# Kernel tuning notes

Measured on AMD Instinct MI355X. Metric: run time of the kernel, lower is better.

## Reference

```python
import jax, jax.numpy as jnp
import numpy as np

D_MODEL = 2048
N_HEADS = 16
HEAD_DIM = D_MODEL // N_HEADS
SEQ = 2048
THETA = 10000.0


def rope_tables(head_dim, context_length, theta=THETA):
    inv_freq = 1.0 / theta ** (jnp.arange(0, head_dim, 2, dtype=jnp.float32) / head_dim)
    angles = jnp.arange(context_length, dtype=jnp.float32)[:, None] * inv_freq[None, :]
    angles = jnp.concatenate([angles, angles], axis=1)  # [S, head_dim]
    return jnp.cos(angles), jnp.sin(angles)


def apply_rope(x, cos, sin):
    # x: [B, H, S, Dh]; cos/sin: [S, Dh]
    half = x.shape[-1] // 2
    x1, x2 = x[..., :half], x[..., half:]
    rotated = jnp.concatenate([-x2, x1], axis=-1)
    return x * cos[None, None] + rotated * sin[None, None]


def setup_inputs() -> dict:
    key = jax.random.key(0)
    ks = jax.random.split(key, 5)
    s = 1.0 / np.sqrt(D_MODEL)
    x = jax.random.normal(ks[0], (2, SEQ, D_MODEL), dtype=jnp.float32)
    Wq = jax.random.normal(ks[1], (D_MODEL, D_MODEL), dtype=jnp.float32) * s
    Wk = jax.random.normal(ks[2], (D_MODEL, D_MODEL), dtype=jnp.float32) * s
    Wv = jax.random.normal(ks[3], (D_MODEL, D_MODEL), dtype=jnp.float32) * s
    Wo = jax.random.normal(ks[4], (D_MODEL, D_MODEL), dtype=jnp.float32) * s
    return {"x": x, "Wq": Wq, "Wk": Wk, "Wv": Wv, "Wo": Wo}


def reference(x, Wq, Wk, Wv, Wo):
    B, S, D = x.shape
    cos, sin = rope_tables(HEAD_DIM, SEQ)
    cos, sin = cos[:S], sin[:S]

    def split_heads(t):  # [B,S,D] -> [B,H,S,Dh]
        return t.reshape(B, S, N_HEADS, HEAD_DIM).transpose(0, 2, 1, 3)

    q = apply_rope(split_heads(x @ Wq.T), cos, sin)
    k = apply_rope(split_heads(x @ Wk.T), cos, sin)
    v = split_heads(x @ Wv.T)

    scores = jnp.einsum('bhqd,bhkd->bhqk', q, k) / np.sqrt(HEAD_DIM).astype(np.float32)
    causal = jnp.tril(jnp.ones((S, S), dtype=bool))
    scores = jnp.where(causal[None, None], scores, -jnp.inf)
    weights = jax.nn.softmax(scores, axis=-1)
    ctx = jnp.einsum('bhqk,bhkd->bhqd', weights, v)
    ctx = ctx.transpose(0, 2, 1, 3).reshape(B, S, D)
    return ctx @ Wo.T
```

## Files before the change

### kernel.cpp

```cpp
#include <hip/hip_runtime.h>
#include <hip/hip_bf16.h>
#include <cstdint>
#include <cstddef>

typedef __bf16 bf16;
typedef __bf16 bf16x4 __attribute__((ext_vector_type(4)));
typedef __bf16 bf16x8 __attribute__((ext_vector_type(8)));
typedef float f32x4 __attribute__((ext_vector_type(4)));

#define D_MODEL 2048
#define SEQ     2048
#define NH      16
#define HD      128
#define BATCH   2
#define QKV_LD  6144

#define SBAR()  __builtin_amdgcn_sched_barrier(0)
#define HWBAR() do { SBAR(); __builtin_amdgcn_s_barrier(); SBAR(); } while (0)

__device__ __forceinline__ void gld16(void* lds, const void* g) {
    __builtin_amdgcn_global_load_lds(
        (const __attribute__((address_space(1))) unsigned int*)g,
        (__attribute__((address_space(3))) unsigned int*)lds,
        16, 0, 0);
}

__global__ __launch_bounds__(256) void cvt_all(const float* __restrict__ x,
                                               const float* __restrict__ Wq,
                                               const float* __restrict__ Wk,
                                               const float* __restrict__ Wv,
                                               const float* __restrict__ Wo,
                                               bf16* __restrict__ out) {
    int i = (blockIdx.x * 256 + threadIdx.x) * 4;
    const float* src;
    int off;
    if (i < 8388608) { src = x; off = i; }
    else {
        int j = i - 8388608;
        int seg = j >> 22;
        src = (seg == 0) ? Wq : (seg == 1) ? Wk : (seg == 2) ? Wv : Wo;
        off = j & 4194303;
    }
    float4 v = *(const float4*)(src + off);
    bf16* o = out + i;
    o[0] = (bf16)v.x; o[1] = (bf16)v.y; o[2] = (bf16)v.z; o[3] = (bf16)v.w;
}

__global__ __launch_bounds__(256) void rope_tables_k(float* __restrict__ cosd,
                                                     float* __restrict__ sind) {
    int id = blockIdx.x * 256 + threadIdx.x;
    int s = id >> 6, d = id & 63;
    float freq = powf(10000.f, -(float)d * (1.f / 64.f));
    float a = (float)s * freq;
    float sn, c;
    sincosf(a, &sn, &c);
    cosd[id] = c;
    sind[id] = sn;
}

__global__ __launch_bounds__(256) void rope_apply(bf16* __restrict__ T,
                                                  const float* __restrict__ cosd,
                                                  const float* __restrict__ sind,
                                                  float scale, int ld) {
    int id = blockIdx.x * 256 + threadIdx.x;
    int row = id >> 10;
    int p = id & 1023;
    int h = p >> 6, d = p & 63;
    int s = row & (SEQ - 1);
    size_t base = (size_t)row * ld + h * HD + d;
    float x1 = (float)T[base];
    float x2 = (float)T[base + 64];
    float c = cosd[(s << 6) + d];
    float sn = sind[(s << 6) + d];
    T[base]      = (bf16)((x1 * c - x2 * sn) * scale);
    T[base + 64] = (bf16)((x2 * c + x1 * sn) * scale);
}

__global__ __launch_bounds__(256) void transpose_v(const bf16* __restrict__ V,
                                                   bf16* __restrict__ Vt, int ld) {
    __shared__ bf16 t[32][33];
    int s0 = blockIdx.x * 32;
    int d0 = blockIdx.y * 32;
    int bh = blockIdx.z;
    int b = bh >> 4, h = bh & 15;
    int tx = threadIdx.x & 31, ty = threadIdx.x >> 5;
#pragma unroll
    for (int i = 0; i < 32; i += 8)
        t[ty + i][tx] = V[((size_t)(b * SEQ + s0 + ty + i)) * ld + h * HD + d0 + tx];
    __syncthreads();
#pragma unroll
    for (int i = 0; i < 32; i += 8)
        Vt[((size_t)bh * HD + d0 + ty + i) * SEQ + s0 + tx] = t[tx][ty + i];
}

template <int OUTF32>
__global__ __launch_bounds__(512, 2)
void gemm8p(const bf16* __restrict__ A, const bf16* __restrict__ B,
            void* __restrict__ Cout, int M, int N, int K) {
    __shared__ __align__(16) bf16 ldsAB[2][2][2][128 * 64];

    const int nM = M >> 8, nN = N >> 8;
    const int cpx = (nM * nN) >> 3;

    int bchm = 0, bchn = 0, best = 0x7fffffff;
    for (int d = 1; d <= cpx; ++d) {
        if (cpx % d) continue;
        int cm = cpx / d;
        if (nM % cm || nN % d) continue;
        if (cm + d < best) { best = cm + d; bchm = cm; bchn = d; }
    }
    int mt0, nt0;
    if (bchm) {
        const int ncn = nN / bchn;
        const int xcd = blockIdx.x & 7, loc = blockIdx.x >> 3;
        mt0 = (xcd / ncn) * bchm + loc / bchn;
        nt0 = (xcd % ncn) * bchn + loc % bchn;
    } else {
        const int lin = (blockIdx.x & 7) * cpx + (blockIdx.x >> 3);
        mt0 = lin / nN; nt0 = lin % nN;
    }
    const int m0 = mt0 * 256, n0 = nt0 * 256;

    const int tid = threadIdx.x;
    const int w = tid >> 6, l = tid & 63;
    const int wm = w >> 2, wn = w & 3;
    const int lg = l >> 4, lc = l & 15;
    const int swz = (lc & 7) << 4;
    const int NT = K >> 6;

    f32x4 acc[2][2][4][2] = {};

    auto stageU = [&](int tau, int u) {
        bf16* dst = &ldsAB[tau & 1][u >> 1][u & 1][0];
        const bf16* src = (u < 2) ? A + (size_t)(m0 + (u & 1) * 128) * K
                                  : B + (size_t)(n0 + (u & 1) * 128) * K;
#pragma unroll
        for (int j = 0; j < 2; ++j) {
            int r = w * 8 + j * 64 + (l >> 3);
            int scb = ((l & 7) * 16) ^ ((r & 7) << 4);
            gld16(dst + (w * 8 + j * 64) * 64, src + (size_t)r * K + tau * 64 + (scb >> 1));
        }
    };

    stageU(0, 0); stageU(0, 1); stageU(0, 2); stageU(0, 3);
    stageU(1, 0); stageU(1, 1);
    SBAR();
    asm volatile("s_waitcnt vmcnt(4)" ::: "memory");
    HWBAR();

    for (int t = 0; t < NT; ++t) {
        const int c = t & 1;
        const char* Ab = (const char*)&ldsAB[c][0][wm][0];
        const char* Bb = (const char*)&ldsAB[c][1][wn >> 1][0];
        const int brow0 = (wn & 1) * 64;
        bf16x8 Af[4][2], Bf[2][2][2];

#pragma unroll
        for (int mt = 0; mt < 4; ++mt)
#pragma unroll
            for (int ks = 0; ks < 2; ++ks)
                Af[mt][ks] = *(const bf16x8*)(Ab + (mt * 16 + lc) * 128 + ((ks * 64 + lg * 16) ^ swz));
#pragma unroll
        for (int nt = 0; nt < 2; ++nt)
#pragma unroll
            for (int ks = 0; ks < 2; ++ks)
                Bf[0][nt][ks] = *(const bf16x8*)(Bb + (brow0 + nt * 16 + lc) * 128 + ((ks * 64 + lg * 16) ^ swz));
        if (t + 1 < NT) stageU(t + 1, 2);
        HWBAR();
        __builtin_amdgcn_s_setprio(1);
#pragma unroll
        for (int mt = 0; mt < 4; ++mt)
#pragma unroll
            for (int nt = 0; nt < 2; ++nt)
#pragma unroll
                for (int ks = 0; ks < 2; ++ks)
                    acc[0][0][mt][nt] = __builtin_amdgcn_mfma_f32_16x16x32_bf16(Af[mt][ks], Bf[0][nt][ks], acc[0][0][mt][nt], 0, 0, 0);
        __builtin_amdgcn_s_setprio(0);
        HWBAR();

#pragma unroll
        for (int nt = 0; nt < 2; ++nt)
#pragma unroll
            for (int ks = 0; ks < 2; ++ks)
                Bf[1][nt][ks] = *(const bf16x8*)(Bb + (brow0 + 32 + nt * 16 + lc) * 128 + ((ks * 64 + lg * 16) ^ swz));
        if (t + 1 < NT) stageU(t + 1, 3);
        HWBAR();
        __builtin_amdgcn_s_setprio(1);
#pragma unroll
        for (int mt = 0; mt < 4; ++mt)
#pragma unroll
            for (int nt = 0; nt < 2; ++nt)
#pragma unroll
                for (int ks = 0; ks < 2; ++ks)
                    acc[0][1][mt][nt] = __builtin_amdgcn_mfma_f32_16x16x32_bf16(Af[mt][ks], Bf[1][nt][ks], acc[0][1][mt][nt], 0, 0, 0);
        __builtin_amdgcn_s_setprio(0);
        HWBAR();

#pragma unroll
        for (int mt = 0; mt < 4; ++mt)
#pragma unroll
            for (int ks = 0; ks < 2; ++ks)
                Af[mt][ks] = *(const bf16x8*)(Ab + (64 + mt * 16 + lc) * 128 + ((ks * 64 + lg * 16) ^ swz));
        HWBAR();
        __builtin_amdgcn_s_setprio(1);
#pragma unroll
        for (int mt = 0; mt < 4; ++mt)
#pragma unroll
            for (int nt = 0; nt < 2; ++nt)
#pragma unroll
                for (int ks = 0; ks < 2; ++ks)
                    acc[1][0][mt][nt] = __builtin_amdgcn_mfma_f32_16x16x32_bf16(Af[mt][ks], Bf[0][nt][ks], acc[1][0][mt][nt], 0, 0, 0);
        __builtin_amdgcn_s_setprio(0);
        HWBAR();

        if (t + 2 < NT) { stageU(t + 2, 0); stageU(t + 2, 1); }
        __builtin_amdgcn_s_setprio(1);
#pragma unroll
        for (int mt = 0; mt < 4; ++mt)
#pragma unroll
            for (int nt = 0; nt < 2; ++nt)
#pragma unroll
                for (int ks = 0; ks < 2; ++ks)
                    acc[1][1][mt][nt] = __builtin_amdgcn_mfma_f32_16x16x32_bf16(Af[mt][ks], Bf[1][nt][ks], acc[1][1][mt][nt], 0, 0, 0);
        __builtin_amdgcn_s_setprio(0);
        SBAR();
        if (t + 2 < NT) asm volatile("s_waitcnt vmcnt(4)" ::: "memory");
        else            asm volatile("s_waitcnt vmcnt(0)" ::: "memory");
        HWBAR();
    }

#pragma unroll
    for (int mq = 0; mq < 2; ++mq)
#pragma unroll
        for (int nq = 0; nq < 2; ++nq)
#pragma unroll
            for (int mt = 0; mt < 4; ++mt)
#pragma unroll
                for (int nt = 0; nt < 2; ++nt)
#pragma unroll
                    for (int rr = 0; rr < 4; ++rr) {
                        size_t row = (size_t)m0 + wm * 128 + mq * 64 + mt * 16 + lg * 4 + rr;
                        size_t col = (size_t)n0 + wn * 64 + nq * 32 + nt * 16 + lc;
                        float v = acc[mq][nq][mt][nt][rr];
                        if (OUTF32) ((float*)Cout)[row * N + col] = v;
                        else        ((bf16*)Cout)[row * N + col] = (bf16)v;
                    }
}

__global__ __launch_bounds__(256)
void flash_attn(const bf16* __restrict__ QKV, const bf16* __restrict__ Vt,
                bf16* __restrict__ O) {
    __shared__ __align__(16) bf16 Ks[2][64 * 128];
    __shared__ __align__(16) bf16 Vs[2][128 * 64];
    __shared__ __align__(16) bf16 p_lds[4][16 * 64];

    const int bid = blockIdx.x;
    const int lin = (bid & 7) * 64 + (bid >> 3);
    const int bh = lin >> 4;
    const int jj = lin & 15;
    const int b = bh >> 4, h = bh & 15;

    const int tid = threadIdx.x;
    const int w = tid >> 6, l = tid & 63;
    const int lg = l >> 4, lc = l & 15;
    const int kswz = (lc & 7) << 4;
    char* pb = (char*)&p_lds[w][0];

    auto stageK = [&](int p, int kb) {
#pragma unroll
        for (int c = 0; c < 4; ++c) {
            int r = c * 16 + w * 4 + (l >> 4);
            int scb = ((l & 15) * 16) ^ ((r & 7) << 4);
            const bf16* g = QKV + ((size_t)(b * SEQ + kb * 64 + r)) * QKV_LD + D_MODEL + h * HD + (scb >> 1);
            gld16(&Ks[p][(c * 16 + w * 4) * 128], g);
        }
    };
    auto stageV = [&](int p, int kb) {
#pragma unroll
        for (int c = 0; c < 4; ++c) {
            int r = c * 32 + w * 8 + (l >> 3);
            int scb = ((l & 7) * 16) ^ ((r & 7) << 4);
            const bf16* g = Vt + ((size_t)bh * HD + r) * SEQ + kb * 64 + (scb >> 1);
            gld16(&Vs[p][(c * 32 + w * 8) * 64], g);
        }
    };

    int cur = 0;
#pragma unroll 1
    for (int ti = 0; ti < 2; ++ti) {
        const int qt = ti ? jj : (31 - jj);
        const int q0 = qt * 64 + w * 16;

        const bf16* qp = QKV + ((size_t)(b * SEQ + q0 + lc)) * QKV_LD + h * HD + lg * 8;
        bf16x8 qf[4];
#pragma unroll
        for (int kc = 0; kc < 4; ++kc) qf[kc] = *(const bf16x8*)(qp + kc * 32);

        f32x4 ctx[8] = {};
        float m_s = -INFINITY, l_s = 0.f;

        stageK(cur, 0);
        stageV(cur, 0);

        for (int kb = 0; kb <= qt; ++kb) {
            __syncthreads();
            if (kb < qt) { stageK(cur ^ 1, kb + 1); stageV(cur ^ 1, kb + 1); }

            const char* kbp = (const char*)&Ks[cur][0];
            f32x4 st[4] = {};
#pragma unroll
            for (int nf = 0; nf < 4; ++nf) {
                int krow = nf * 16 + lc;
#pragma unroll
                for (int kc = 0; kc < 4; ++kc) {
                    bf16x8 kf = *(const bf16x8*)(kbp + krow * 256 + ((kc * 64 + lg * 16) ^ kswz));
                    st[nf] = __builtin_amdgcn_mfma_f32_16x16x32_bf16(kf, qf[kc], st[nf], 0, 0, 0);
                }
            }

            if (kb == qt) {
                int q = q0 + lc;
#pragma unroll
                for (int nf = 0; nf < 4; ++nf) {
                    int key = kb * 64 + nf * 16 + lg * 4;
#pragma unroll
                    for (int r = 0; r < 4; ++r)
                        if (key + r > q) st[nf][r] = -INFINITY;
                }
            }

            float mx = -INFINITY;
#pragma unroll
            for (int nf = 0; nf < 4; ++nf)
#pragma unroll
                for (int r = 0; r < 4; ++r) mx = fmaxf(mx, st[nf][r]);
            mx = fmaxf(mx, __shfl_xor(mx, 16));
            mx = fmaxf(mx, __shfl_xor(mx, 32));
            float mi = fmaxf(m_s, mx);
            float scv = __expf(m_s - mi);
            m_s = mi;

            float rs = 0.f;
#pragma unroll
            for (int nf = 0; nf < 4; ++nf) {
                float p0 = __expf(st[nf][0] - mi);
                float p1 = __expf(st[nf][1] - mi);
                float p2 = __expf(st[nf][2] - mi);
                float p3 = __expf(st[nf][3] - mi);
                rs += (p0 + p1) + (p2 + p3);
                bf16x4 pv = { (bf16)p0, (bf16)p1, (bf16)p2, (bf16)p3 };
                *(bf16x4*)(pb + lc * 128 + ((nf * 32 + lg * 8) ^ kswz)) = pv;
            }
            rs += __shfl_xor(rs, 16);
            rs += __shfl_xor(rs, 32);
            l_s = l_s * scv + rs;

            float scvr[4];
#pragma unroll
            for (int r = 0; r < 4; ++r) scvr[r] = __shfl(scv, lg * 4 + r);
#pragma unroll
            for (int nd = 0; nd < 8; ++nd)
#pragma unroll
                for (int r = 0; r < 4; ++r) ctx[nd][r] *= scvr[r];

            asm volatile("s_waitcnt lgkmcnt(0)" ::: "memory");
            SBAR();
            bf16x8 pa0 = *(const bf16x8*)(pb + lc * 128 + ((lg * 16) ^ kswz));
            bf16x8 pa1 = *(const bf16x8*)(pb + lc * 128 + ((64 + lg * 16) ^ kswz));

            const char* vb = (const char*)&Vs[cur][0];
#pragma unroll
            for (int nd = 0; nd < 8; ++nd) {
                int vrow = nd * 16 + lc;
#pragma unroll
                for (int k2 = 0; k2 < 2; ++k2) {
                    bf16x8 vf = *(const bf16x8*)(vb + vrow * 128 + ((k2 * 64 + lg * 16) ^ kswz));
                    ctx[nd] = __builtin_amdgcn_mfma_f32_16x16x32_bf16(k2 ? pa1 : pa0, vf, ctx[nd], 0, 0, 0);
                }
            }
            cur ^= 1;
        }

        float lr[4];
#pragma unroll
        for (int r = 0; r < 4; ++r) lr[r] = 1.f / __shfl(l_s, lg * 4 + r);
#pragma unroll
        for (int nd = 0; nd < 8; ++nd)
#pragma unroll
            for (int r = 0; r < 4; ++r)
                O[((size_t)(b * SEQ + q0 + lg * 4 + r)) * D_MODEL + h * HD + nd * 16 + lc] =
                    (bf16)(ctx[nd][r] * lr[r]);
    }
}

extern "C" void kernel_launch(void* const* d_in, const int* in_sizes, int n_in,
                              void* d_out, int out_size, void* d_ws, size_t ws_size,
                              hipStream_t stream) {
    const float* x  = (const float*)d_in[0];
    const float* Wq = (const float*)d_in[1];
    const float* Wk = (const float*)d_in[2];
    const float* Wv = (const float*)d_in[3];
    const float* Wo = (const float*)d_in[4];

    char* ws = (char*)d_ws;
    bf16* xb   = (bf16*)(ws + 0);
    bf16* wqkv = (bf16*)(ws + 16777216);
    bf16* wob  = (bf16*)(ws + 41943040);
    bf16* QKV  = (bf16*)(ws + 50331648);
    bf16* Vtb  = (bf16*)(ws + 100663296);
    float* cosd = (float*)(ws + 117440512);
    float* sind = (float*)(ws + 117964800);

    cvt_all<<<25165824 / 1024, 256, 0, stream>>>(x, Wq, Wk, Wv, Wo, xb);

    rope_tables_k<<<(SEQ * 64) / 256, 256, 0, stream>>>(cosd, sind);

    gemm8p<0><<<dim3((QKV_LD / 256) * ((BATCH * SEQ) / 256)), 512, 0, stream>>>(
        xb, wqkv, QKV, BATCH * SEQ, QKV_LD, D_MODEL);

    const float qscale = 0.08838834764831845f;
    rope_apply<<<(BATCH * SEQ * 1024) / 256, 256, 0, stream>>>(QKV,           cosd, sind, qscale, QKV_LD);
    rope_apply<<<(BATCH * SEQ * 1024) / 256, 256, 0, stream>>>(QKV + D_MODEL, cosd, sind, 1.0f,   QKV_LD);

    transpose_v<<<dim3(SEQ / 32, HD / 32, BATCH * NH), 256, 0, stream>>>(QKV + 2 * D_MODEL, Vtb, QKV_LD);

    flash_attn<<<dim3(512), 256, 0, stream>>>(QKV, Vtb, xb );

    gemm8p<1><<<dim3((D_MODEL / 256) * ((BATCH * SEQ) / 256)), 512, 0, stream>>>(
        xb, wob, d_out, BATCH * SEQ, D_MODEL, D_MODEL);
}
```

Before: 311.0 us.

## Fuse V transpose into QKV GEMM epilogue and deepen load pipeline

```diff
diff --git a/kernel.cpp b/kernel.cpp
--- a/kernel.cpp
+++ b/kernel.cpp
@@ -76,49 +76,16 @@
     T[base + 64] = (bf16)((x2 * c + x1 * sn) * scale);
 }
 
-__global__ __launch_bounds__(256) void transpose_v(const bf16* __restrict__ V,
-                                                   bf16* __restrict__ Vt, int ld) {
-    __shared__ bf16 t[32][33];
-    int s0 = blockIdx.x * 32;
-    int d0 = blockIdx.y * 32;
-    int bh = blockIdx.z;
-    int b = bh >> 4, h = bh & 15;
-    int tx = threadIdx.x & 31, ty = threadIdx.x >> 5;
-#pragma unroll
-    for (int i = 0; i < 32; i += 8)
-        t[ty + i][tx] = V[((size_t)(b * SEQ + s0 + ty + i)) * ld + h * HD + d0 + tx];
-    __syncthreads();
-#pragma unroll
-    for (int i = 0; i < 32; i += 8)
-        Vt[((size_t)bh * HD + d0 + ty + i) * SEQ + s0 + tx] = t[tx][ty + i];
-}
-
-template <int OUTF32>
+template <int OUTMODE>
 __global__ __launch_bounds__(512, 2)
 void gemm8p(const bf16* __restrict__ A, const bf16* __restrict__ B,
-            void* __restrict__ Cout, int M, int N, int K) {
+            void* __restrict__ Cout, bf16* __restrict__ Vt,
+            int M, int N, int K, int chm, int chn, int ncn) {
     __shared__ __align__(16) bf16 ldsAB[2][2][2][128 * 64];
 
-    const int nM = M >> 8, nN = N >> 8;
-    const int cpx = (nM * nN) >> 3;
-
-    int bchm = 0, bchn = 0, best = 0x7fffffff;
-    for (int d = 1; d <= cpx; ++d) {
-        if (cpx % d) continue;
-        int cm = cpx / d;
-        if (nM % cm || nN % d) continue;
-        if (cm + d < best) { best = cm + d; bchm = cm; bchn = d; }
-    }
-    int mt0, nt0;
-    if (bchm) {
-        const int ncn = nN / bchn;
-        const int xcd = blockIdx.x & 7, loc = blockIdx.x >> 3;
-        mt0 = (xcd / ncn) * bchm + loc / bchn;
-        nt0 = (xcd % ncn) * bchn + loc % bchn;
-    } else {
-        const int lin = (blockIdx.x & 7) * cpx + (blockIdx.x >> 3);
-        mt0 = lin / nN; nt0 = lin % nN;
-    }
+    const int xcd = blockIdx.x & 7, loc = blockIdx.x >> 3;
+    const int mt0 = (xcd / ncn) * chm + loc / chn;
+    const int nt0 = (xcd % ncn) * chn + loc % chn;
     const int m0 = mt0 * 256, n0 = nt0 * 256;
 
     const int tid = threadIdx.x;
@@ -127,25 +94,27 @@
     const int lg = l >> 4, lc = l & 15;
     const int swz = (lc & 7) << 4;
     const int NT = K >> 6;
+    const int HMAX = NT * 4;
 
     f32x4 acc[2][2][4][2] = {};
 
-    auto stageU = [&](int tau, int u) {
-        bf16* dst = &ldsAB[tau & 1][u >> 1][u & 1][0];
-        const bf16* src = (u < 2) ? A + (size_t)(m0 + (u & 1) * 128) * K
-                                  : B + (size_t)(n0 + (u & 1) * 128) * K;
+    auto stage = [&](int H) {
+        const int tau = H >> 2, h = H & 3;
+        bf16* dst = &ldsAB[tau & 1][h >> 1][h & 1][0];
 #pragma unroll
         for (int j = 0; j < 2; ++j) {
             int r = w * 8 + j * 64 + (l >> 3);
             int scb = ((l & 7) * 16) ^ ((r & 7) << 4);
-            gld16(dst + (w * 8 + j * 64) * 64, src + (size_t)r * K + tau * 64 + (scb >> 1));
+            const bf16* g = (h < 2)
+                ? A + (size_t)(m0 + (h & 1) * 128 + r) * K + tau * 64 + (scb >> 1)
+                : B + (size_t)(n0 + (h & 1) * 128 + r) * K + tau * 64 + (scb >> 1);
+            gld16(dst + (w * 8 + j * 64) * 64, g);
         }
     };
 
-    stageU(0, 0); stageU(0, 1); stageU(0, 2); stageU(0, 3);
-    stageU(1, 0); stageU(1, 1);
+    stage(0); stage(1); stage(2); stage(3); stage(4);
     SBAR();
-    asm volatile("s_waitcnt vmcnt(4)" ::: "memory");
+    asm volatile("s_waitcnt vmcnt(2)" ::: "memory");
     HWBAR();
 
     for (int t = 0; t < NT; ++t) {
@@ -165,7 +134,7 @@
 #pragma unroll
             for (int ks = 0; ks < 2; ++ks)
                 Bf[0][nt][ks] = *(const bf16x8*)(Bb + (brow0 + nt * 16 + lc) * 128 + ((ks * 64 + lg * 16) ^ swz));
-        if (t + 1 < NT) stageU(t + 1, 2);
+        { int H = 4 * t + 5; if (H < HMAX) stage(H); }
         HWBAR();
         __builtin_amdgcn_s_setprio(1);
 #pragma unroll
@@ -183,7 +152,7 @@
 #pragma unroll
             for (int ks = 0; ks < 2; ++ks)
                 Bf[1][nt][ks] = *(const bf16x8*)(Bb + (brow0 + 32 + nt * 16 + lc) * 128 + ((ks * 64 + lg * 16) ^ swz));
-        if (t + 1 < NT) stageU(t + 1, 3);
+        { int H = 4 * t + 6; if (H < HMAX) stage(H); }
         HWBAR();
         __builtin_amdgcn_s_setprio(1);
 #pragma unroll
@@ -201,6 +170,7 @@
 #pragma unroll
             for (int ks = 0; ks < 2; ++ks)
                 Af[mt][ks] = *(const bf16x8*)(Ab + (64 + mt * 16 + lc) * 128 + ((ks * 64 + lg * 16) ^ swz));
+        { int H = 4 * t + 7; if (H < HMAX) stage(H); }
         HWBAR();
         __builtin_amdgcn_s_setprio(1);
 #pragma unroll
@@ -213,7 +183,8 @@
         __builtin_amdgcn_s_setprio(0);
         HWBAR();
 
-        if (t + 2 < NT) { stageU(t + 2, 0); stageU(t + 2, 1); }
+        { int H = 4 * t + 8; if (H < HMAX) stage(H); }
+        HWBAR();
         __builtin_amdgcn_s_setprio(1);
 #pragma unroll
         for (int mt = 0; mt < 4; ++mt)
@@ -224,11 +195,12 @@
                     acc[1][1][mt][nt] = __builtin_amdgcn_mfma_f32_16x16x32_bf16(Af[mt][ks], Bf[1][nt][ks], acc[1][1][mt][nt], 0, 0, 0);
         __builtin_amdgcn_s_setprio(0);
         SBAR();
-        if (t + 2 < NT) asm volatile("s_waitcnt vmcnt(4)" ::: "memory");
+        if (t + 2 < NT) asm volatile("s_waitcnt vmcnt(2)" ::: "memory");
         else            asm volatile("s_waitcnt vmcnt(0)" ::: "memory");
         HWBAR();
     }
 
+    const bool vregion = (OUTMODE == 2) && (n0 >= 2 * D_MODEL);
 #pragma unroll
     for (int mq = 0; mq < 2; ++mq)
 #pragma unroll
@@ -236,15 +208,26 @@
 #pragma unroll
             for (int mt = 0; mt < 4; ++mt)
 #pragma unroll
-                for (int nt = 0; nt < 2; ++nt)
-#pragma unroll
-                    for (int rr = 0; rr < 4; ++rr) {
-                        size_t row = (size_t)m0 + wm * 128 + mq * 64 + mt * 16 + lg * 4 + rr;
-                        size_t col = (size_t)n0 + wn * 64 + nq * 32 + nt * 16 + lc;
-                        float v = acc[mq][nq][mt][nt][rr];
-                        if (OUTF32) ((float*)Cout)[row * N + col] = v;
-                        else        ((bf16*)Cout)[row * N + col] = (bf16)v;
+                for (int nt = 0; nt < 2; ++nt) {
+                    size_t row0 = (size_t)m0 + wm * 128 + mq * 64 + mt * 16 + lg * 4;
+                    size_t col  = (size_t)n0 + wn * 64 + nq * 32 + nt * 16 + lc;
+                    if (vregion) {
+                        int col4 = (int)col - 2 * D_MODEL;
+                        int h = col4 >> 7, d = col4 & 127;
+                        int b = (int)(row0 >> 11), s0 = (int)(row0 & 2047);
+                        bf16x4 pv;
+#pragma unroll
+                        for (int rr = 0; rr < 4; ++rr) pv[rr] = (bf16)acc[mq][nq][mt][nt][rr];
+                        *(bf16x4*)(Vt + ((size_t)(b * NH + h) * HD + d) * SEQ + s0) = pv;
+                    } else {
+#pragma unroll
+                        for (int rr = 0; rr < 4; ++rr) {
+                            float v = acc[mq][nq][mt][nt][rr];
+                            if (OUTMODE == 1) ((float*)Cout)[(row0 + rr) * N + col] = v;
+                            else              ((bf16*)Cout)[(row0 + rr) * N + col] = (bf16)v;
+                        }
                     }
+                }
 }
 
 __global__ __launch_bounds__(256)
@@ -415,17 +398,15 @@
 
     rope_tables_k<<<(SEQ * 64) / 256, 256, 0, stream>>>(cosd, sind);
 
-    gemm8p<0><<<dim3((QKV_LD / 256) * ((BATCH * SEQ) / 256)), 512, 0, stream>>>(
-        xb, wqkv, QKV, BATCH * SEQ, QKV_LD, D_MODEL);
+    gemm8p<2><<<dim3(384), 512, 0, stream>>>(
+        xb, wqkv, QKV, Vtb, BATCH * SEQ, QKV_LD, D_MODEL, 8, 6, 4);
 
     const float qscale = 0.08838834764831845f;
     rope_apply<<<(BATCH * SEQ * 1024) / 256, 256, 0, stream>>>(QKV,           cosd, sind, qscale, QKV_LD);
     rope_apply<<<(BATCH * SEQ * 1024) / 256, 256, 0, stream>>>(QKV + D_MODEL, cosd, sind, 1.0f,   QKV_LD);
 
-    transpose_v<<<dim3(SEQ / 32, HD / 32, BATCH * NH), 256, 0, stream>>>(QKV + 2 * D_MODEL, Vtb, QKV_LD);
-
     flash_attn<<<dim3(512), 256, 0, stream>>>(QKV, Vtb, xb );
 
-    gemm8p<1><<<dim3((D_MODEL / 256) * ((BATCH * SEQ) / 256)), 512, 0, stream>>>(
-        xb, wob, d_out, BATCH * SEQ, D_MODEL, D_MODEL);
-}
+    gemm8p<1><<<dim3(128), 512, 0, stream>>>(
+        xb, wob, d_out, nullptr, BATCH * SEQ, D_MODEL, D_MODEL, 4, 4, 2);
+}
```

After: 293.7 us. 5.6% less time.

## Shrink GEMM block tile to 128x256 and simplify XCD tile mapping

Applied to the files above, without the earlier changes.

```diff
diff --git a/kernel.cpp b/kernel.cpp
--- a/kernel.cpp
+++ b/kernel.cpp
@@ -95,31 +95,15 @@
 
 template <int OUTF32>
 __global__ __launch_bounds__(512, 2)
-void gemm8p(const bf16* __restrict__ A, const bf16* __restrict__ B,
-            void* __restrict__ Cout, int M, int N, int K) {
-    __shared__ __align__(16) bf16 ldsAB[2][2][2][128 * 64];
-
-    const int nM = M >> 8, nN = N >> 8;
-    const int cpx = (nM * nN) >> 3;
-
-    int bchm = 0, bchn = 0, best = 0x7fffffff;
-    for (int d = 1; d <= cpx; ++d) {
-        if (cpx % d) continue;
-        int cm = cpx / d;
-        if (nM % cm || nN % d) continue;
-        if (cm + d < best) { best = cm + d; bchm = cm; bchn = d; }
-    }
-    int mt0, nt0;
-    if (bchm) {
-        const int ncn = nN / bchn;
-        const int xcd = blockIdx.x & 7, loc = blockIdx.x >> 3;
-        mt0 = (xcd / ncn) * bchm + loc / bchn;
-        nt0 = (xcd % ncn) * bchn + loc % bchn;
-    } else {
-        const int lin = (blockIdx.x & 7) * cpx + (blockIdx.x >> 3);
-        mt0 = lin / nN; nt0 = lin % nN;
-    }
-    const int m0 = mt0 * 256, n0 = nt0 * 256;
+void gemm128(const bf16* __restrict__ A, const bf16* __restrict__ B,
+             void* __restrict__ Cout, int M, int N, int K) {
+    __shared__ __align__(16) bf16 ldsA[2][128 * 64];
+    __shared__ __align__(16) bf16 ldsB[2][2][128 * 64];
+
+    const int nN = N >> 8;
+    const int cpx = gridDim.x >> 3;
+    const int lin = (blockIdx.x & 7) * cpx + (blockIdx.x >> 3);
+    const int m0 = (lin / nN) * 128, n0 = (lin % nN) * 256;
 
     const int tid = threadIdx.x;
     const int w = tid >> 6, l = tid & 63;
@@ -128,44 +112,50 @@
     const int swz = (lc & 7) << 4;
     const int NT = K >> 6;
 
-    f32x4 acc[2][2][4][2] = {};
-
-    auto stageU = [&](int tau, int u) {
-        bf16* dst = &ldsAB[tau & 1][u >> 1][u & 1][0];
-        const bf16* src = (u < 2) ? A + (size_t)(m0 + (u & 1) * 128) * K
-                                  : B + (size_t)(n0 + (u & 1) * 128) * K;
+    f32x4 acc[2][4][2] = {};
+
+    auto stageA = [&](int tau) {
+        bf16* dst = &ldsA[tau & 1][0];
 #pragma unroll
         for (int j = 0; j < 2; ++j) {
-            int r = w * 8 + j * 64 + (l >> 3);
+            int r = w * 16 + j * 8 + (l >> 3);
             int scb = ((l & 7) * 16) ^ ((r & 7) << 4);
-            gld16(dst + (w * 8 + j * 64) * 64, src + (size_t)r * K + tau * 64 + (scb >> 1));
+            gld16(dst + (w * 16 + j * 8) * 64, A + (size_t)(m0 + r) * K + tau * 64 + (scb >> 1));
         }
     };
-
-    stageU(0, 0); stageU(0, 1); stageU(0, 2); stageU(0, 3);
-    stageU(1, 0); stageU(1, 1);
+    auto stageB = [&](int tau, int u) {
+        bf16* dst = &ldsB[tau & 1][u][0];
+#pragma unroll
+        for (int j = 0; j < 2; ++j) {
+            int r = w * 16 + j * 8 + (l >> 3);
+            int scb = ((l & 7) * 16) ^ ((r & 7) << 4);
+            gld16(dst + (w * 16 + j * 8) * 64, B + (size_t)(n0 + u * 128 + r) * K + tau * 64 + (scb >> 1));
+        }
+    };
+
+    stageA(0); stageB(0, 0); stageB(0, 1); stageA(1);
     SBAR();
-    asm volatile("s_waitcnt vmcnt(4)" ::: "memory");
+    asm volatile("s_waitcnt vmcnt(2)" ::: "memory");
     HWBAR();
 
     for (int t = 0; t < NT; ++t) {
         const int c = t & 1;
-        const char* Ab = (const char*)&ldsAB[c][0][wm][0];
-        const char* Bb = (const char*)&ldsAB[c][1][wn >> 1][0];
+        const char* Ab = (const char*)&ldsA[c][0];
+        const char* Bb = (const char*)&ldsB[c][wn >> 1][0];
         const int brow0 = (wn & 1) * 64;
-        bf16x8 Af[4][2], Bf[2][2][2];
+        bf16x8 Af[4][2], Bf[2][2];
 
 #pragma unroll
         for (int mt = 0; mt < 4; ++mt)
 #pragma unroll
             for (int ks = 0; ks < 2; ++ks)
-                Af[mt][ks] = *(const bf16x8*)(Ab + (mt * 16 + lc) * 128 + ((ks * 64 + lg * 16) ^ swz));
+                Af[mt][ks] = *(const bf16x8*)(Ab + (wm * 64 + mt * 16 + lc) * 128 + ((ks * 64 + lg * 16) ^ swz));
 #pragma unroll
         for (int nt = 0; nt < 2; ++nt)
 #pragma unroll
             for (int ks = 0; ks < 2; ++ks)
-                Bf[0][nt][ks] = *(const bf16x8*)(Bb + (brow0 + nt * 16 + lc) * 128 + ((ks * 64 + lg * 16) ^ swz));
-        if (t + 1 < NT) stageU(t + 1, 2);
+                Bf[nt][ks] = *(const bf16x8*)(Bb + (brow0 + nt * 16 + lc) * 128 + ((ks * 64 + lg * 16) ^ swz));
+        if (t + 1 < NT) stageB(t + 1, 0);
         HWBAR();
         __builtin_amdgcn_s_setprio(1);
 #pragma unroll
@@ -174,7 +164,7 @@
             for (int nt = 0; nt < 2; ++nt)
 #pragma unroll
                 for (int ks = 0; ks < 2; ++ks)
-                    acc[0][0][mt][nt] = __builtin_amdgcn_mfma_f32_16x16x32_bf16(Af[mt][ks], Bf[0][nt][ks], acc[0][0][mt][nt], 0, 0, 0);
+                    acc[0][mt][nt] = __builtin_amdgcn_mfma_f32_16x16x32_bf16(Af[mt][ks], Bf[nt][ks], acc[0][mt][nt], 0, 0, 0);
         __builtin_amdgcn_s_setprio(0);
         HWBAR();
 
@@ -182,8 +172,9 @@
         for (int nt = 0; nt < 2; ++nt)
 #pragma unroll
             for (int ks = 0; ks < 2; ++ks)
-                Bf[1][nt][ks] = *(const bf16x8*)(Bb + (brow0 + 32 + nt * 16 + lc) * 128 + ((ks * 64 + lg * 16) ^ swz));
-        if (t + 1 < NT) stageU(t + 1, 3);
+                Bf[nt][ks] = *(const bf16x8*)(Bb + (brow0 + 32 + nt * 16 + lc) * 128 + ((ks * 64 + lg * 16) ^ swz));
+        if (t + 1 < NT) stageB(t + 1, 1);
+        if (t + 2 < NT) stageA(t + 2);
         HWBAR();
         __builtin_amdgcn_s_setprio(1);
 #pragma unroll
@@ -192,59 +183,28 @@
             for (int nt = 0; nt < 2; ++nt)
 #pragma unroll
                 for (int ks = 0; ks < 2; ++ks)
-                    acc[0][1][mt][nt] = __builtin_amdgcn_mfma_f32_16x16x32_bf16(Af[mt][ks], Bf[1][nt][ks], acc[0][1][mt][nt], 0, 0, 0);
-        __builtin_amdgcn_s_setprio(0);
-        HWBAR();
-
-#pragma unroll
-        for (int mt = 0; mt < 4; ++mt)
-#pragma unroll
-            for (int ks = 0; ks < 2; ++ks)
-                Af[mt][ks] = *(const bf16x8*)(Ab + (64 + mt * 16 + lc) * 128 + ((ks * 64 + lg * 16) ^ swz));
-        HWBAR();
-        __builtin_amdgcn_s_setprio(1);
-#pragma unroll
-        for (int mt = 0; mt < 4; ++mt)
-#pragma unroll
-            for (int nt = 0; nt < 2; ++nt)
-#pragma unroll
-                for (int ks = 0; ks < 2; ++ks)
-                    acc[1][0][mt][nt] = __builtin_amdgcn_mfma_f32_16x16x32_bf16(Af[mt][ks], Bf[0][nt][ks], acc[1][0][mt][nt], 0, 0, 0);
-        __builtin_amdgcn_s_setprio(0);
-        HWBAR();
-
-        if (t + 2 < NT) { stageU(t + 2, 0); stageU(t + 2, 1); }
-        __builtin_amdgcn_s_setprio(1);
-#pragma unroll
-        for (int mt = 0; mt < 4; ++mt)
-#pragma unroll
-            for (int nt = 0; nt < 2; ++nt)
-#pragma unroll
-                for (int ks = 0; ks < 2; ++ks)
-                    acc[1][1][mt][nt] = __builtin_amdgcn_mfma_f32_16x16x32_bf16(Af[mt][ks], Bf[1][nt][ks], acc[1][1][mt][nt], 0, 0, 0);
+                    acc[1][mt][nt] = __builtin_amdgcn_mfma_f32_16x16x32_bf16(Af[mt][ks], Bf[nt][ks], acc[1][mt][nt], 0, 0, 0);
         __builtin_amdgcn_s_setprio(0);
         SBAR();
-        if (t + 2 < NT) asm volatile("s_waitcnt vmcnt(4)" ::: "memory");
+        if (t + 2 < NT) asm volatile("s_waitcnt vmcnt(2)" ::: "memory");
         else            asm volatile("s_waitcnt vmcnt(0)" ::: "memory");
         HWBAR();
     }
 
 #pragma unroll
-    for (int mq = 0; mq < 2; ++mq)
-#pragma unroll
-        for (int nq = 0; nq < 2; ++nq)
-#pragma unroll
-            for (int mt = 0; mt < 4; ++mt)
-#pragma unroll
-                for (int nt = 0; nt < 2; ++nt)
-#pragma unroll
-                    for (int rr = 0; rr < 4; ++rr) {
-                        size_t row = (size_t)m0 + wm * 128 + mq * 64 + mt * 16 + lg * 4 + rr;
-                        size_t col = (size_t)n0 + wn * 64 + nq * 32 + nt * 16 + lc;
-                        float v = acc[mq][nq][mt][nt][rr];
-                        if (OUTF32) ((float*)Cout)[row * N + col] = v;
-                        else        ((bf16*)Cout)[row * N + col] = (bf16)v;
-                    }
+    for (int nq = 0; nq < 2; ++nq)
+#pragma unroll
+        for (int mt = 0; mt < 4; ++mt)
+#pragma unroll
+            for (int nt = 0; nt < 2; ++nt)
+#pragma unroll
+                for (int rr = 0; rr < 4; ++rr) {
+                    size_t row = (size_t)m0 + wm * 64 + mt * 16 + lg * 4 + rr;
+                    size_t col = (size_t)n0 + wn * 64 + nq * 32 + nt * 16 + lc;
+                    float v = acc[nq][mt][nt][rr];
+                    if (OUTF32) ((float*)Cout)[row * N + col] = v;
+                    else        ((bf16*)Cout)[row * N + col] = (bf16)v;
+                }
 }
 
 __global__ __launch_bounds__(256)
@@ -415,7 +375,7 @@
 
     rope_tables_k<<<(SEQ * 64) / 256, 256, 0, stream>>>(cosd, sind);
 
-    gemm8p<0><<<dim3((QKV_LD / 256) * ((BATCH * SEQ) / 256)), 512, 0, stream>>>(
+    gemm128<0><<<dim3(768), 512, 0, stream>>>(
         xb, wqkv, QKV, BATCH * SEQ, QKV_LD, D_MODEL);
 
     const float qscale = 0.08838834764831845f;
@@ -426,6 +386,6 @@
 
     flash_attn<<<dim3(512), 256, 0, stream>>>(QKV, Vtb, xb );
 
-    gemm8p<1><<<dim3((D_MODEL / 256) * ((BATCH * SEQ) / 256)), 512, 0, stream>>>(
+    gemm128<1><<<dim3(256), 512, 0, stream>>>(
         xb, wob, d_out, BATCH * SEQ, D_MODEL, D_MODEL);
 }
```

Measured after the change: 276.3 us. 11.1% less time.
